# Kernel tuning notes

Hardware: AMD Instinct MI355X
Metric: run time of the kernel (lower is better)

The kernel has to match this reference:

```python
import jax, jax.numpy as jnp
import numpy as np

B, T, E, H = 2, 2048, 1024, 16  # batch, seq(block_size), n_embed, n_head


def setup_inputs() -> dict:
    key = jax.random.key(0)
    kx, kq, kk, kv, kf = jax.random.split(key, 5)
    s = 0.02
    return {
        "x": jax.random.normal(kx, (B, T, E), jnp.float32),
        "Wq": jax.random.normal(kq, (E, E), jnp.float32) * s,
        "Wk": jax.random.normal(kk, (E, E), jnp.float32) * s,
        "Wv": jax.random.normal(kv, (E, E), jnp.float32) * s,
        "Wf": jax.random.normal(kf, (E, E), jnp.float32) * s,
        "bf": jnp.zeros((E,), jnp.float32),
    }


def reference(x, Wq, Wk, Wv, Wf, bf):
    b, t, e = x.shape
    dh = e // H
    # per-head projections (no bias), heads concatenated along feature dim
    q = (x @ Wq).reshape(b, t, H, dh)
    k = (x @ Wk).reshape(b, t, H, dh)
    v = (x @ Wv).reshape(b, t, H, dh)
    # NOTE: original scales by sqrt(full embed dim C), not sqrt(head_size)
    scores = jnp.einsum("bqhd,bkhd->bhqk", q, k) / jnp.sqrt(jnp.asarray(e, x.dtype))
    causal = jnp.tril(jnp.ones((t, t), bool))
    scores = jnp.where(causal, scores, -jnp.inf)
    wei = jax.nn.softmax(scores, axis=-1)
    attn = jnp.einsum("bhqk,bkhd->bqhd", wei, v).reshape(b, t, e)
    x = x + attn  # residual (no out-projection in original)
    # FeedForward: single Linear + ReLU, residual
    return x + jnp.maximum(x @ Wf + bf, 0)
```

## Files before the change

### kernel.cpp

```cpp
#include <hip/hip_runtime.h>
#include <cstdint>
#include <cstddef>

typedef unsigned short u16;
typedef short short8 __attribute__((ext_vector_type(8)));
typedef float floatx4 __attribute__((ext_vector_type(4)));

__device__ __forceinline__ float bf2f(u16 u) {
    union { unsigned int i; float f; } v; v.i = ((unsigned int)u) << 16; return v.f;
}
__device__ __forceinline__ u16 f2bf(float f) {
    union { float f; unsigned int i; } v; v.f = f;
    unsigned int u = v.i;
    return (u16)((u + 0x7fffu + ((u >> 16) & 1u)) >> 16);
}

#if __has_builtin(__builtin_amdgcn_exp2f)
#define EXP2F(x) __builtin_amdgcn_exp2f(x)
#else
#define EXP2F(x) exp2f(x)
#endif

__device__ __forceinline__ void gload_lds16(const u16* g, void* lds_wave_base) {
    __builtin_amdgcn_global_load_lds(
        (__attribute__((address_space(1))) void*)g,
        (__attribute__((address_space(3))) void*)lds_wave_base,
        16, 0, 0);
}

__global__ void conv_transpose_k(const float* __restrict__ w0, const float* __restrict__ w1,
                                 const float* __restrict__ w2, const float* __restrict__ w3,
                                 u16* __restrict__ o0, u16* __restrict__ o1,
                                 u16* __restrict__ o2, u16* __restrict__ o3, int n) {
    __shared__ float t[32][33];
    const float* w; u16* o;
    switch (blockIdx.z) {
        case 0: w = w0; o = o0; break;
        case 1: w = w1; o = o1; break;
        case 2: w = w2; o = o2; break;
        default: w = w3; o = o3; break;
    }
    int tx = threadIdx.x, ty = threadIdx.y;
    int x0 = blockIdx.x * 32, y0 = blockIdx.y * 32;
    t[ty][tx] = w[(size_t)(y0 + ty) * n + x0 + tx];
    __syncthreads();
    o[(size_t)(x0 + ty) * n + y0 + tx] = f2bf(t[tx][ty]);
}

__global__ void conv_k(const float* __restrict__ in, u16* __restrict__ out, int n) {
    int i = (blockIdx.x * blockDim.x + threadIdx.x) * 4;
    if (i >= n) return;
    float4 v = *(const float4*)&in[i];
    ushort4 o;
    o.x = f2bf(v.x); o.y = f2bf(v.y); o.z = f2bf(v.z); o.w = f2bf(v.w);
    *(ushort4*)&out[i] = o;
}

__global__ void vpack_k(const u16* __restrict__ vbd, u16* __restrict__ vp, int T) {
    __shared__ u16 t[32][33];
    int bh = blockIdx.z;
    int t0 = blockIdx.x * 32, d0 = blockIdx.y * 32;
    int tx = threadIdx.x, ty = threadIdx.y;
    t[ty][tx] = vbd[((size_t)bh * T + t0 + ty) * 64 + d0 + tx];
    __syncthreads();
    int kblk = t0 >> 6, tbase = t0 & 32;
    vp[(((size_t)bh * (T / 64) + kblk) * 64 + d0 + ty) * 64 + tbase + tx] = t[tx][ty];
}

__global__ __launch_bounds__(256) void gemm_qkv(
    const u16* __restrict__ A, const u16* __restrict__ Bt,
    u16* __restrict__ qpk, u16* __restrict__ kpk, u16* __restrict__ vbd,
    int M, int T, int K) {
    __shared__ u16 lds_a[128][32];
    __shared__ u16 lds_b[128][32];

    const int tid = threadIdx.x;
    const int lane = tid & 63, wave = tid >> 6;
    const int wm = (wave >> 1) * 64, wn = (wave & 1) * 64;
    const int bm = blockIdx.x * 128, bn = blockIdx.y * 128;
    const int l15 = lane & 15, lq = lane >> 4;

    const int sec = bn >> 10;
    u16* dst = (sec == 0) ? qpk : (sec == 1) ? kpk : vbd;
    const int bnE = bn & 1023;

    floatx4 acc[4][4];
#pragma unroll
    for (int i = 0; i < 4; ++i)
#pragma unroll
        for (int j = 0; j < 4; ++j) acc[i][j] = (floatx4)0.0f;

    for (int k0 = 0; k0 < K; k0 += 32) {
#pragma unroll
        for (int it = 0; it < 2; ++it) {
            int idx = it * 256 + tid;
            int row = idx >> 2;
            int c8 = (idx & 3) * 8;
            size_t ldsoff = (size_t)(it * 256 + wave * 64) * 16;
            gload_lds16(&A[(size_t)(bm + row) * K + k0 + c8], (char*)&lds_a[0][0] + ldsoff);
            gload_lds16(&Bt[(size_t)(bn + row) * K + k0 + c8], (char*)&lds_b[0][0] + ldsoff);
        }
        __syncthreads();

        short8 af[4], bfr[4];
#pragma unroll
        for (int i = 0; i < 4; ++i) af[i] = *(const short8*)&lds_a[wm + i * 16 + l15][lq * 8];
#pragma unroll
        for (int j = 0; j < 4; ++j) bfr[j] = *(const short8*)&lds_b[wn + j * 16 + l15][lq * 8];

#pragma unroll
        for (int i = 0; i < 4; ++i)
#pragma unroll
            for (int j = 0; j < 4; ++j)
                acc[i][j] = __builtin_amdgcn_mfma_f32_16x16x32_bf16(af[i], bfr[j], acc[i][j], 0, 0, 0);
        __syncthreads();
    }

#pragma unroll
    for (int i = 0; i < 4; ++i)
#pragma unroll
        for (int j = 0; j < 4; ++j)
#pragma unroll
            for (int r = 0; r < 4; ++r) {
                int row = bm + wm + i * 16 + lq * 4 + r;
                int colE = bnE + wn + j * 16 + l15;
                int h = colE >> 6, d = colE & 63;
                int b = row >> 11, t = row & 2047;
                dst[(((size_t)(b * 16 + h) * T) + t) * 64 + d] = f2bf(acc[i][j][r]);
            }
}

__global__ __launch_bounds__(256) void gemm64_bt(
    const u16* __restrict__ A, const u16* __restrict__ Bt, float* __restrict__ Cf,
    const float* __restrict__ bias, const u16* __restrict__ resid,
    int M, int N, int K) {
    __shared__ u16 lds_a[64][32];
    __shared__ u16 lds_b[128][32];

    const int tid = threadIdx.x;
    const int lane = tid & 63, wave = tid >> 6;
    const int wm = (wave >> 1) * 32, wn = (wave & 1) * 64;
    const int bm = blockIdx.x * 64, bn = blockIdx.y * 128;
    const int l15 = lane & 15, lq = lane >> 4;

    floatx4 acc[2][4];
#pragma unroll
    for (int i = 0; i < 2; ++i)
#pragma unroll
        for (int j = 0; j < 4; ++j) acc[i][j] = (floatx4)0.0f;

    for (int k0 = 0; k0 < K; k0 += 32) {
        {
            int row = tid >> 2;
            int c8 = (tid & 3) * 8;
            size_t ldsoff = (size_t)(wave * 64) * 16;
            gload_lds16(&A[(size_t)(bm + row) * K + k0 + c8], (char*)&lds_a[0][0] + ldsoff);
        }
#pragma unroll
        for (int it = 0; it < 2; ++it) {
            int idx = it * 256 + tid;
            int row = idx >> 2;
            int c8 = (idx & 3) * 8;
            size_t ldsoff = (size_t)(it * 256 + wave * 64) * 16;
            gload_lds16(&Bt[(size_t)(bn + row) * K + k0 + c8], (char*)&lds_b[0][0] + ldsoff);
        }
        __syncthreads();

        short8 af[2], bfr[4];
#pragma unroll
        for (int i = 0; i < 2; ++i) af[i] = *(const short8*)&lds_a[wm + i * 16 + l15][lq * 8];
#pragma unroll
        for (int j = 0; j < 4; ++j) bfr[j] = *(const short8*)&lds_b[wn + j * 16 + l15][lq * 8];

#pragma unroll
        for (int i = 0; i < 2; ++i)
#pragma unroll
            for (int j = 0; j < 4; ++j)
                acc[i][j] = __builtin_amdgcn_mfma_f32_16x16x32_bf16(af[i], bfr[j], acc[i][j], 0, 0, 0);
        __syncthreads();
    }

#pragma unroll
    for (int i = 0; i < 2; ++i)
#pragma unroll
        for (int j = 0; j < 4; ++j)
#pragma unroll
            for (int r = 0; r < 4; ++r) {
                int row = bm + wm + i * 16 + lq * 4 + r;
                int col = bn + wn + j * 16 + l15;
                float v = acc[i][j][r];
                v = fmaxf(v + bias[col], 0.0f) + bf2f(resid[(size_t)row * N + col]);
                Cf[(size_t)row * N + col] = v;
            }
}

#define STAGE(KT, BUF)                                                            \
    {                                                                             \
        const u16* kc_ = kb + (size_t)((KT) * 64 + r0) * 64 + swz0;               \
        gload_lds16(kc_, (char*)kbuf + (BUF) * 8192 + wave * 1024);               \
        gload_lds16(kc_ + 32 * 64, (char*)kbuf + (BUF) * 8192 + 4096 + wave * 1024); \
        const u16* vc_ = vp + (size_t)(KT) * 4096 + r0 * 64 + swz0;               \
        gload_lds16(vc_, (char*)vbuf + (BUF) * 8192 + wave * 1024);               \
        gload_lds16(vc_ + 32 * 64, (char*)vbuf + (BUF) * 8192 + 4096 + wave * 1024); \
    }

__global__ __launch_bounds__(256) void attn10_k(
    const u16* __restrict__ qpk, const u16* __restrict__ kpk,
    const u16* __restrict__ vpack, const float* __restrict__ xf,
    u16* __restrict__ y, int T, int E) {
    __shared__ u16 kbuf[2][64 * 64];
    __shared__ u16 vbuf[2][64 * 64];

    const int tid = threadIdx.x;
    const int lane = tid & 63, wave = tid >> 6;
    const int l15 = lane & 15, lq = lane >> 4;
    const int bh = blockIdx.x;
    const int b = bh >> 4, h = bh & 15;
    const int qb = 31 - (int)blockIdx.y;

    const u16* qp = qpk + (size_t)bh * T * 64;
    const u16* kb = kpk + (size_t)bh * T * 64;
    const u16* vp = vpack + (size_t)bh * T * 64;

    const float c2 = 0.04508422f;
    const int r0 = tid >> 3;
    const int slot = tid & 7;
    const int fr0 = (r0 & 3) | (((r0 >> 3) & 1) << 2);
    const int swz0 = ((slot - fr0) & 7) * 8;

    const int rbase = ((l15 >> 2) * 8) + (l15 & 3);
    const int sA = lq + (l15 & 7);
    const int sB = lq + ((l15 & 3) | (((l15 >> 3) & 1) << 2));

    const int qt = qb * 64 + wave * 16;
    const int qg = qt + l15;
    const int nkb = qb + 1;

    short8 aq[2];
#pragma unroll
    for (int c = 0; c < 2; ++c)
        aq[c] = *(const short8*)&qp[(size_t)qg * 64 + c * 32 + lq * 8];

    floatx4 o[4];
#pragma unroll
    for (int n = 0; n < 4; ++n) o[n] = (floatx4)0.0f;
    float lsum = 0.0f;

    STAGE(0, 0);
    __syncthreads();

#pragma unroll 1
    for (int kt = 0; kt < nkb; ++kt) {
        const int kc0 = kt * 64;
        const int cur = kt & 1;
        const int curoff = cur * 8192;

        if (kt + 1 < nkb) STAGE(kt + 1, cur ^ 1);

        floatx4 st[4];
#pragma unroll
        for (int t2 = 0; t2 < 4; ++t2) {
            const int row = rbase + (t2 & 1) * 4 + (t2 >> 1) * 32;
            floatx4 sa = (floatx4)0.0f;
#pragma unroll
            for (int c = 0; c < 2; ++c) {
                int off = row * 128 + ((c * 4 + sA) & 7) * 16;
                short8 bk = *(const short8*)((const char*)kbuf + curoff + off);
                sa = __builtin_amdgcn_mfma_f32_16x16x32_bf16(bk, aq[c], sa, 0, 0, 0);
            }
            st[t2] = sa;
        }

        const bool partial = (kt == qb);
        unsigned int pw[8];
#pragma unroll
        for (int t2 = 0; t2 < 4; ++t2) {
            float e0, e1, e2, e3;
            const int kg0 = kc0 + lq * 8 + (t2 & 1) * 4 + ((t2 >> 1) * 32);
            if (partial) {
                e0 = (kg0 + 0 <= qg) ? EXP2F(st[t2][0] * c2) : 0.0f;
                e1 = (kg0 + 1 <= qg) ? EXP2F(st[t2][1] * c2) : 0.0f;
                e2 = (kg0 + 2 <= qg) ? EXP2F(st[t2][2] * c2) : 0.0f;
                e3 = (kg0 + 3 <= qg) ? EXP2F(st[t2][3] * c2) : 0.0f;
            } else {
                e0 = EXP2F(st[t2][0] * c2);
                e1 = EXP2F(st[t2][1] * c2);
                e2 = EXP2F(st[t2][2] * c2);
                e3 = EXP2F(st[t2][3] * c2);
            }
            lsum += (e0 + e1) + (e2 + e3);
            unsigned int w0, w1;
            asm("v_cvt_pk_bf16_f32 %0, %1, %2" : "=v"(w0) : "v"(e0), "v"(e1));
            asm("v_cvt_pk_bf16_f32 %0, %1, %2" : "=v"(w1) : "v"(e2), "v"(e3));
            pw[t2 * 2 + 0] = w0;
            pw[t2 * 2 + 1] = w1;
        }

#pragma unroll
        for (int kc = 0; kc < 2; ++kc) {
            union { unsigned int u[4]; short8 s; } ap;
            ap.u[0] = pw[kc * 4 + 0];
            ap.u[1] = pw[kc * 4 + 1];
            ap.u[2] = pw[kc * 4 + 2];
            ap.u[3] = pw[kc * 4 + 3];
#pragma unroll
            for (int n = 0; n < 4; ++n) {
                int off = (n * 16 + l15) * 128 + ((kc * 4 + sB) & 7) * 16;
                short8 bv = *(const short8*)((const char*)vbuf + curoff + off);
                o[n] = __builtin_amdgcn_mfma_f32_16x16x32_bf16(ap.s, bv, o[n], 0, 0, 0);
            }
        }
        __syncthreads();
    }

    lsum += __shfl_xor(lsum, 16, 64);
    lsum += __shfl_xor(lsum, 32, 64);

    const float* xp = xf + (size_t)b * T * E + (size_t)h * 64;
    u16* yp = y + (size_t)b * T * E + (size_t)h * 64;
    float rl[4];
#pragma unroll
    for (int r = 0; r < 4; ++r) rl[r] = 1.0f / __shfl(lsum, lq * 4 + r, 64);
#pragma unroll
    for (int n = 0; n < 4; ++n)
#pragma unroll
        for (int r = 0; r < 4; ++r) {
            int rowg = qt + lq * 4 + r;
            int col = n * 16 + l15;
            float val = o[n][r] * rl[r];
            float res = __builtin_nontemporal_load(xp + (size_t)rowg * E + col);
            yp[(size_t)rowg * E + col] = f2bf(res + val);
        }
}

extern "C" void kernel_launch(void* const* d_in, const int* in_sizes, int n_in,
                              void* d_out, int out_size, void* d_ws, size_t ws_size,
                              hipStream_t stream) {
    const int B = 2, T = 2048, E = 1024;
    const int M = B * T;

    const float* x  = (const float*)d_in[0];
    const float* Wq = (const float*)d_in[1];
    const float* Wk = (const float*)d_in[2];
    const float* Wv = (const float*)d_in[3];
    const float* Wf = (const float*)d_in[4];
    const float* bf = (const float*)d_in[5];
    float* out = (float*)d_out;

    u16* ws = (u16*)d_ws;
    const size_t WN = (size_t)E * E;
    const size_t XN = (size_t)M * E;
    u16* Wqkv  = ws;
    u16* WfT   = ws + 3 * WN;
    u16* xb    = ws + 4 * WN;
    u16* qpk   = ws + 4 * WN + XN;
    u16* kpk   = ws + 4 * WN + 2 * XN;
    u16* vbd   = ws + 4 * WN + 3 * XN;
    u16* yb    = ws + 4 * WN + 4 * XN;
    u16* vpack = xb;

    conv_transpose_k<<<dim3(E / 32, E / 32, 4), dim3(32, 32), 0, stream>>>(
        Wq, Wk, Wv, Wf, Wqkv, Wqkv + WN, Wqkv + 2 * WN, WfT, E);
    conv_k<<<(int)(XN / 1024), 256, 0, stream>>>(x, xb, (int)XN);

    gemm_qkv<<<dim3(M / 128, 3 * E / 128), 256, 0, stream>>>(
        xb, Wqkv, qpk, kpk, vbd, M, T, E);

    vpack_k<<<dim3(T / 32, 2, B * 16), dim3(32, 32), 0, stream>>>(vbd, vpack, T);

    attn10_k<<<dim3(B * 16, T / 64), 256, 0, stream>>>(qpk, kpk, vpack, x, yb, T, E);

    gemm64_bt<<<dim3(M / 64, E / 128), 256, 0, stream>>>(yb, WfT, out, bf, yb, M, E, E);
}
```

Before: 193.1 us.

## Double-buffer GEMM LDS loads, fuse V packing into QKV epilogue, add MFMA priority

Both GEMM kernels now stage K-tiles into double-buffered LDS so the next tile's global-to-LDS load overlaps the current MFMAs. The QKV GEMM epilogue goes through a swizzled LDS tile and writes 16-byte vectors. For the V section it writes the transposed, packed layout directly, which removes the separate vpack kernel and its round trip through global memory. The attention kernel raises wave priority around its MFMA blocks with s_setprio. The cost is more LDS per block, which may lower occupancy, plus extra syncs in the epilogue.

```diff
diff --git a/kernel.cpp b/kernel.cpp
--- a/kernel.cpp
+++ b/kernel.cpp
@@ -56,23 +56,26 @@
     *(ushort4*)&out[i] = o;
 }
 
-__global__ void vpack_k(const u16* __restrict__ vbd, u16* __restrict__ vp, int T) {
-    __shared__ u16 t[32][33];
-    int bh = blockIdx.z;
-    int t0 = blockIdx.x * 32, d0 = blockIdx.y * 32;
-    int tx = threadIdx.x, ty = threadIdx.y;
-    t[ty][tx] = vbd[((size_t)bh * T + t0 + ty) * 64 + d0 + tx];
-    __syncthreads();
-    int kblk = t0 >> 6, tbase = t0 & 32;
-    vp[(((size_t)bh * (T / 64) + kblk) * 64 + d0 + ty) * 64 + tbase + tx] = t[tx][ty];
-}
+#define QSTG(K0, BUF)                                                          \
+    {                                                                          \
+        _Pragma("unroll")                                                      \
+        for (int it = 0; it < 2; ++it) {                                       \
+            int idx = it * 256 + tid;                                          \
+            int row = idx >> 2;                                                \
+            int c8 = (idx & 3) * 8;                                            \
+            size_t ldsoff = (size_t)(it * 256 + wave * 64) * 16;               \
+            gload_lds16(&A[(size_t)(bm + row) * K + (K0) + c8],                \
+                        (char*)smem + (BUF) * 8192 + ldsoff);                  \
+            gload_lds16(&Bt[(size_t)(bn + row) * K + (K0) + c8],               \
+                        (char*)smem + 16384 + (BUF) * 8192 + ldsoff);          \
+        }                                                                      \
+    }
 
 __global__ __launch_bounds__(256) void gemm_qkv(
     const u16* __restrict__ A, const u16* __restrict__ Bt,
-    u16* __restrict__ qpk, u16* __restrict__ kpk, u16* __restrict__ vbd,
+    u16* __restrict__ qpk, u16* __restrict__ kpk, u16* __restrict__ vpk,
     int M, int T, int K) {
-    __shared__ u16 lds_a[128][32];
-    __shared__ u16 lds_b[128][32];
+    __shared__ __align__(16) u16 smem[16384];
 
     const int tid = threadIdx.x;
     const int lane = tid & 63, wave = tid >> 6;
@@ -81,7 +84,7 @@
     const int l15 = lane & 15, lq = lane >> 4;
 
     const int sec = bn >> 10;
-    u16* dst = (sec == 0) ? qpk : (sec == 1) ? kpk : vbd;
+    u16* dst = (sec == 0) ? qpk : (sec == 1) ? kpk : vpk;
     const int bnE = bn & 1023;
 
     floatx4 acc[4][4];
@@ -90,23 +93,21 @@
 #pragma unroll
         for (int j = 0; j < 4; ++j) acc[i][j] = (floatx4)0.0f;
 
-    for (int k0 = 0; k0 < K; k0 += 32) {
-#pragma unroll
-        for (int it = 0; it < 2; ++it) {
-            int idx = it * 256 + tid;
-            int row = idx >> 2;
-            int c8 = (idx & 3) * 8;
-            size_t ldsoff = (size_t)(it * 256 + wave * 64) * 16;
-            gload_lds16(&A[(size_t)(bm + row) * K + k0 + c8], (char*)&lds_a[0][0] + ldsoff);
-            gload_lds16(&Bt[(size_t)(bn + row) * K + k0 + c8], (char*)&lds_b[0][0] + ldsoff);
-        }
-        __syncthreads();
-
+    const int nkt = K / 32;
+    QSTG(0, 0);
+    __syncthreads();
+
+    for (int kt = 0; kt < nkt; ++kt) {
+        const int cur = kt & 1;
+        if (kt + 1 < nkt) QSTG((kt + 1) * 32, cur ^ 1);
+
+        const u16* la = smem + cur * 4096;
+        const u16* lb = smem + 8192 + cur * 4096;
         short8 af[4], bfr[4];
 #pragma unroll
-        for (int i = 0; i < 4; ++i) af[i] = *(const short8*)&lds_a[wm + i * 16 + l15][lq * 8];
-#pragma unroll
-        for (int j = 0; j < 4; ++j) bfr[j] = *(const short8*)&lds_b[wn + j * 16 + l15][lq * 8];
+        for (int i = 0; i < 4; ++i) af[i] = *(const short8*)&la[(wm + i * 16 + l15) * 32 + lq * 8];
+#pragma unroll
+        for (int j = 0; j < 4; ++j) bfr[j] = *(const short8*)&lb[(wn + j * 16 + l15) * 32 + lq * 8];
 
 #pragma unroll
         for (int i = 0; i < 4; ++i)
@@ -116,26 +117,91 @@
         __syncthreads();
     }
 
-#pragma unroll
-    for (int i = 0; i < 4; ++i)
-#pragma unroll
-        for (int j = 0; j < 4; ++j)
+    if (sec < 2) {
+#pragma unroll
+        for (int i = 0; i < 4; ++i)
 #pragma unroll
             for (int r = 0; r < 4; ++r) {
-                int row = bm + wm + i * 16 + lq * 4 + r;
-                int colE = bnE + wn + j * 16 + l15;
+                int trow = wm + i * 16 + lq * 4 + r;
+                int s7 = ((trow >> 2) & 7) << 4;
+#pragma unroll
+                for (int j = 0; j < 4; ++j) {
+                    int col = wn + j * 16 + l15;
+                    smem[trow * 128 + (col ^ s7)] = f2bf(acc[i][j][r]);
+                }
+            }
+        __syncthreads();
+        const int rg = tid >> 3, cc = tid & 7;
+#pragma unroll
+        for (int p = 0; p < 4; ++p)
+#pragma unroll
+            for (int sfx = 0; sfx < 2; ++sfx) {
+                int row = p * 32 + rg;
+                int ch = cc + sfx * 8;
+                short8 v = *(const short8*)&smem[row * 128 + ((ch * 8) ^ (((row >> 2) & 7) << 4))];
+                int colE = bnE + ch * 8;
                 int h = colE >> 6, d = colE & 63;
-                int b = row >> 11, t = row & 2047;
-                dst[(((size_t)(b * 16 + h) * T) + t) * 64 + d] = f2bf(acc[i][j][r]);
-            }
-}
+                int rowg = bm + row;
+                int b = rowg >> 11, t = rowg & 2047;
+                *(short8*)&dst[(((size_t)(b * 16 + h) * T) + t) * 64 + d] = v;
+            }
+    } else {
+#pragma unroll
+        for (int j = 0; j < 4; ++j) {
+            int clo = wn + j * 16 + l15;
+            int s7 = ((clo >> 2) & 7) << 4;
+#pragma unroll
+            for (int i = 0; i < 4; ++i)
+#pragma unroll
+                for (int r = 0; r < 4; ++r) {
+                    int trow = wm + i * 16 + lq * 4 + r;
+                    smem[clo * 128 + (trow ^ s7)] = f2bf(acc[i][j][r]);
+                }
+        }
+        __syncthreads();
+        const int rg = tid >> 3, cc = tid & 7;
+        const int b = bm >> 11;
+#pragma unroll
+        for (int p = 0; p < 4; ++p)
+#pragma unroll
+            for (int sfx = 0; sfx < 2; ++sfx) {
+                int clo = p * 32 + rg;
+                int ch = cc + sfx * 8;
+                short8 v = *(const short8*)&smem[clo * 128 + ((ch * 8) ^ (((clo >> 2) & 7) << 4))];
+                int colE = bnE + clo;
+                int h = colE >> 6, d = colE & 63;
+                int t = (bm + ch * 8) & 2047;
+                int kblk = t >> 6, tloc = t & 63;
+                *(short8*)&dst[(((size_t)(b * 16 + h) * 32 + kblk) * 64 + d) * 64 + tloc] = v;
+            }
+    }
+}
+
+#define FSTG(K0, BUF)                                                          \
+    {                                                                          \
+        {                                                                      \
+            int row = tid >> 2;                                                \
+            int c8 = (tid & 3) * 8;                                            \
+            size_t ldsoff = (size_t)(wave * 64) * 16;                          \
+            gload_lds16(&A[(size_t)(bm + row) * K + (K0) + c8],                \
+                        (char*)smemF + (BUF) * 4096 + ldsoff);                 \
+        }                                                                      \
+        _Pragma("unroll")                                                      \
+        for (int it = 0; it < 2; ++it) {                                       \
+            int idx = it * 256 + tid;                                          \
+            int row = idx >> 2;                                                \
+            int c8 = (idx & 3) * 8;                                            \
+            size_t ldsoff = (size_t)(it * 256 + wave * 64) * 16;               \
+            gload_lds16(&Bt[(size_t)(bn + row) * K + (K0) + c8],               \
+                        (char*)smemF + 8192 + (BUF) * 8192 + ldsoff);          \
+        }                                                                      \
+    }
 
 __global__ __launch_bounds__(256) void gemm64_bt(
     const u16* __restrict__ A, const u16* __restrict__ Bt, float* __restrict__ Cf,
     const float* __restrict__ bias, const u16* __restrict__ resid,
     int M, int N, int K) {
-    __shared__ u16 lds_a[64][32];
-    __shared__ u16 lds_b[128][32];
+    __shared__ __align__(16) u16 smemF[12288];
 
     const int tid = threadIdx.x;
     const int lane = tid & 63, wave = tid >> 6;
@@ -149,28 +215,21 @@
 #pragma unroll
         for (int j = 0; j < 4; ++j) acc[i][j] = (floatx4)0.0f;
 
-    for (int k0 = 0; k0 < K; k0 += 32) {
-        {
-            int row = tid >> 2;
-            int c8 = (tid & 3) * 8;
-            size_t ldsoff = (size_t)(wave * 64) * 16;
-            gload_lds16(&A[(size_t)(bm + row) * K + k0 + c8], (char*)&lds_a[0][0] + ldsoff);
-        }
-#pragma unroll
-        for (int it = 0; it < 2; ++it) {
-            int idx = it * 256 + tid;
-            int row = idx >> 2;
-            int c8 = (idx & 3) * 8;
-            size_t ldsoff = (size_t)(it * 256 + wave * 64) * 16;
-            gload_lds16(&Bt[(size_t)(bn + row) * K + k0 + c8], (char*)&lds_b[0][0] + ldsoff);
-        }
-        __syncthreads();
-
+    const int nkt = K / 32;
+    FSTG(0, 0);
+    __syncthreads();
+
+    for (int kt = 0; kt < nkt; ++kt) {
+        const int cur = kt & 1;
+        if (kt + 1 < nkt) FSTG((kt + 1) * 32, cur ^ 1);
+
+        const u16* la = smemF + cur * 2048;
+        const u16* lb = smemF + 4096 + cur * 2048 * 2;
         short8 af[2], bfr[4];
 #pragma unroll
-        for (int i = 0; i < 2; ++i) af[i] = *(const short8*)&lds_a[wm + i * 16 + l15][lq * 8];
-#pragma unroll
-        for (int j = 0; j < 4; ++j) bfr[j] = *(const short8*)&lds_b[wn + j * 16 + l15][lq * 8];
+        for (int i = 0; i < 2; ++i) af[i] = *(const short8*)&la[(wm + i * 16 + l15) * 32 + lq * 8];
+#pragma unroll
+        for (int j = 0; j < 4; ++j) bfr[j] = *(const short8*)&lb[(wn + j * 16 + l15) * 32 + lq * 8];
 
 #pragma unroll
         for (int i = 0; i < 2; ++i)
@@ -258,6 +317,7 @@
         if (kt + 1 < nkb) STAGE(kt + 1, cur ^ 1);
 
         floatx4 st[4];
+        __builtin_amdgcn_s_setprio(1);
 #pragma unroll
         for (int t2 = 0; t2 < 4; ++t2) {
             const int row = rbase + (t2 & 1) * 4 + (t2 >> 1) * 32;
@@ -270,6 +330,7 @@
             }
             st[t2] = sa;
         }
+        __builtin_amdgcn_s_setprio(0);
 
         const bool partial = (kt == qb);
         unsigned int pw[8];
@@ -296,6 +357,7 @@
             pw[t2 * 2 + 1] = w1;
         }
 
+        __builtin_amdgcn_s_setprio(1);
 #pragma unroll
         for (int kc = 0; kc < 2; ++kc) {
             union { unsigned int u[4]; short8 s; } ap;
@@ -310,6 +372,7 @@
                 o[n] = __builtin_amdgcn_mfma_f32_16x16x32_bf16(ap.s, bv, o[n], 0, 0, 0);
             }
         }
+        __builtin_amdgcn_s_setprio(0);
         __syncthreads();
     }
 
@@ -355,20 +418,17 @@
     u16* xb    = ws + 4 * WN;
     u16* qpk   = ws + 4 * WN + XN;
     u16* kpk   = ws + 4 * WN + 2 * XN;
-    u16* vbd   = ws + 4 * WN + 3 * XN;
+    u16* vpk   = ws + 4 * WN + 3 * XN;
     u16* yb    = ws + 4 * WN + 4 * XN;
-    u16* vpack = xb;
 
     conv_transpose_k<<<dim3(E / 32, E / 32, 4), dim3(32, 32), 0, stream>>>(
         Wq, Wk, Wv, Wf, Wqkv, Wqkv + WN, Wqkv + 2 * WN, WfT, E);
     conv_k<<<(int)(XN / 1024), 256, 0, stream>>>(x, xb, (int)XN);
 
     gemm_qkv<<<dim3(M / 128, 3 * E / 128), 256, 0, stream>>>(
-        xb, Wqkv, qpk, kpk, vbd, M, T, E);
-
-    vpack_k<<<dim3(T / 32, 2, B * 16), dim3(32, 32), 0, stream>>>(vbd, vpack, T);
-
-    attn10_k<<<dim3(B * 16, T / 64), 256, 0, stream>>>(qpk, kpk, vpack, x, yb, T, E);
+        xb, Wqkv, qpk, kpk, vpk, M, T, E);
+
+    attn10_k<<<dim3(B * 16, T / 64), 256, 0, stream>>>(qpk, kpk, vpk, x, yb, T, E);
 
     gemm64_bt<<<dim3(M / 64, E / 128), 256, 0, stream>>>(yb, WfT, out, bf, yb, M, E, E);
 }
```

New measurement: 183.8 us. -4.9%, faster.
